# Kernel optimization log

Measured on AMD Instinct MI355X. Metric: run time of the kernel, lower is better.

Reference implementation:

```python
import jax, jax.numpy as jnp
import numpy as np

D_MODEL = 1024
NUM_HEADS = 16
D_K = D_MODEL // NUM_HEADS
SIM_THRESH = 0.7


def setup_inputs() -> dict:
    key = jax.random.key(0)
    ks = jax.random.split(key, 7)
    bs, seq = 2, 2048
    scale = 1.0 / np.sqrt(D_MODEL)
    x = jax.random.normal(ks[0], (bs, seq, D_MODEL), dtype=jnp.float32)
    Wq = jax.random.normal(ks[1], (D_MODEL, D_MODEL), dtype=jnp.float32) * scale
    Wk = jax.random.normal(ks[2], (D_MODEL, D_MODEL), dtype=jnp.float32) * scale
    Wv = jax.random.normal(ks[3], (D_MODEL, D_MODEL), dtype=jnp.float32) * scale
    bq = jax.random.normal(ks[4], (D_MODEL,), dtype=jnp.float32) * scale
    bk = jax.random.normal(ks[5], (D_MODEL,), dtype=jnp.float32) * scale
    bv = jax.random.normal(ks[6], (D_MODEL,), dtype=jnp.float32) * scale
    return {"x": x, "Wq": Wq, "bq": bq, "Wk": Wk, "bk": bk, "Wv": Wv, "bv": bv}


def reference(x, Wq, bq, Wk, bk, Wv, bv):
    bs, seq, d_model = x.shape
    # dynamic structural mask: cosine similarity > 0.7, shared across heads
    norm_x = x / jnp.maximum(jnp.linalg.norm(x, axis=-1, keepdims=True), 1e-12)
    sim = jnp.einsum('bsd,btd->bst', norm_x, norm_x)          # [B,S,S]
    mask = (sim > SIM_THRESH)[:, None, :, :]                  # [B,1,S,S]

    def proj(W, b):
        y = x @ W.T + b                                        # [B,S,D]
        return y.reshape(bs, seq, NUM_HEADS, D_K).transpose(0, 2, 1, 3)  # [B,H,S,dk]

    q = proj(Wq, bq)
    k = proj(Wk, bk)
    v = proj(Wv, bv)

    scores = jnp.einsum('bhsd,bhtd->bhst', q, k) / jnp.sqrt(jnp.float32(D_K))
    scores = jnp.where(mask, scores, -jnp.inf)
    attn = jax.nn.softmax(scores, axis=-1)                     # diag always unmasked
    return jnp.einsum('bhst,bhtd->bhsd', attn, v)              # [B,H,S,dk]
```

## Files before the change

kernel.cpp:

```cpp
#include <hip/hip_runtime.h>
#include <stdint.h>
#include <math.h>

#define D_MODEL 1024
#define NUM_HEADS 16
#define D_K 64
#define SEQ 2048
#define BATCH 2
#define SIM_THRESH 0.7f

#define TS 64
#define BK 32
#define NIT (D_MODEL / BK)

#define NROWS (BATCH * SEQ)
#define VP_BLOCKS ((NROWS / TS) * (D_MODEL / TS))
#define SIM_ROWB (SEQ / TS)
#define SIM_TRI (SIM_ROWB * (SIM_ROWB + 1) / 2)
#define SIM_BLOCKS (SIM_TRI * BATCH)
#define GRID (VP_BLOCKS + SIM_BLOCKS)

#define TILE_SH (TS * BK)

typedef __attribute__((ext_vector_type(8))) short bf16x8;
typedef __attribute__((ext_vector_type(4))) float f32x4;

static __device__ __forceinline__ unsigned short f2bf(float f) {
    unsigned int u = __float_as_uint(f);
    unsigned int r = (u + 0x7FFF + ((u >> 16) & 1)) >> 16;
    return (unsigned short)r;
}
static __device__ __forceinline__ float bf2f(unsigned short u) {
    return __uint_as_float(((unsigned int)u) << 16);
}

__global__ __launch_bounds__(256) void k_prep(const float* __restrict__ x,
                                              const float* __restrict__ Wv,
                                              unsigned short* __restrict__ xn,
                                              unsigned short* __restrict__ Wvb,
                                              float* __restrict__ norms,
                                              int* __restrict__ cnt) {
    int bid = blockIdx.x, tid = threadIdx.x;
    if (bid < NROWS) {
        const float4* xr = (const float4*)(x + (size_t)bid * D_MODEL);
        float4 vv = xr[tid];
        float ss = vv.x * vv.x + vv.y * vv.y + vv.z * vv.z + vv.w * vv.w;
        for (int off = 32; off > 0; off >>= 1) ss += __shfl_down(ss, off, 64);
        __shared__ float wsum[4];
        int lane = tid & 63, wv = tid >> 6;
        if (lane == 0) wsum[wv] = ss;
        __syncthreads();
        float nrm = sqrtf(wsum[0] + wsum[1] + wsum[2] + wsum[3]);
        float inv = 1.0f / fmaxf(nrm, 1e-12f);
        ushort4 o;
        o.x = f2bf(vv.x * inv); o.y = f2bf(vv.y * inv);
        o.z = f2bf(vv.z * inv); o.w = f2bf(vv.w * inv);
        *(ushort4*)(xn + (size_t)bid * D_MODEL + tid * 4) = o;
        if (tid == 0) { norms[bid] = nrm; cnt[bid] = 0; }
    } else {
        size_t i = (size_t)(bid - NROWS) * 256 + tid;
        float4 w = ((const float4*)Wv)[i];
        ushort4 o;
        o.x = f2bf(w.x); o.y = f2bf(w.y); o.z = f2bf(w.z); o.w = f2bf(w.w);
        *(ushort4*)(Wvb + i * 4) = o;
    }
}

static __device__ __forceinline__ void stage64x32(const unsigned short* __restrict__ gsrc,
                                                  int rowBase, int kk,
                                                  short* ldsDst, int tid) {
    int row = tid >> 2;
    int ch  = tid & 3;
    const unsigned short* ga = gsrc + (size_t)(rowBase + row) * D_MODEL + kk + ch * 8;
    __builtin_amdgcn_global_load_lds(
        (const __attribute__((address_space(1))) unsigned int*)ga,
        (__attribute__((address_space(3))) unsigned int*)(ldsDst + tid * 8),
        16, 0, 0);
}

__global__ __launch_bounds__(256) void k_main(const unsigned short* __restrict__ xn,
                                              const unsigned short* __restrict__ Wvb,
                                              const float* __restrict__ bv,
                                              const float* __restrict__ norms,
                                              float* __restrict__ v,
                                              int* __restrict__ cnt,
                                              float* __restrict__ out) {
    __shared__ short As[2 * TILE_SH];
    __shared__ short Bs[2 * TILE_SH];
    int bid = blockIdx.x;
    int tid = threadIdx.x;
    int lane = tid & 63, wave = tid >> 6;
    int wm = wave & 1, wn = wave >> 1;
    int lrow = lane & 15, quad = lane >> 4;

    const unsigned short* Asrc;
    const unsigned short* Bsrc;
    int rowBase, colBase;
    bool isV;
    int b = 0, bi = 0, bj = 0;
    if (bid < VP_BLOCKS) {
        isV = true;
        rowBase = (bid >> 4) * TS;
        colBase = (bid & 15) * TS;
        Asrc = xn;
        Bsrc = Wvb;
    } else {
        isV = false;
        int sidx = bid - VP_BLOCKS;
        b = (sidx >= SIM_TRI) ? 1 : 0;
        int r = sidx - b * SIM_TRI;
        bi = 0;
        while (r >= SIM_ROWB - bi) { r -= SIM_ROWB - bi; ++bi; }
        bj = bi + r;
        rowBase = bi * TS;
        colBase = bj * TS;
        Asrc = xn + (size_t)b * SEQ * D_MODEL;
        Bsrc = Asrc;
    }

    int aoff[2], boff[2];
#pragma unroll
    for (int i = 0; i < 2; ++i) {
        aoff[i] = (wm * 32 + i * 16 + lrow) * BK + quad * 8;
        boff[i] = (wn * 32 + i * 16 + lrow) * BK + quad * 8;
    }
    f32x4 acc[2][2] = {};

    stage64x32(Asrc, rowBase, 0, As, tid);
    stage64x32(Bsrc, colBase, 0, Bs, tid);
    __syncthreads();
    for (int it = 0; it < NIT; ++it) {
        int cur = it & 1, nxt = cur ^ 1;
        if (it + 1 < NIT) {
            stage64x32(Asrc, rowBase, (it + 1) * BK, As + nxt * TILE_SH, tid);
            stage64x32(Bsrc, colBase, (it + 1) * BK, Bs + nxt * TILE_SH, tid);
        }
        const short* Ac = As + cur * TILE_SH;
        const short* Bc = Bs + cur * TILE_SH;
        bf16x8 av[2], bvv[2];
#pragma unroll
        for (int i = 0; i < 2; ++i) av[i]  = *(const bf16x8*)(Ac + aoff[i]);
#pragma unroll
        for (int i = 0; i < 2; ++i) bvv[i] = *(const bf16x8*)(Bc + boff[i]);
#pragma unroll
        for (int mt = 0; mt < 2; ++mt)
#pragma unroll
            for (int nt = 0; nt < 2; ++nt)
                acc[mt][nt] = __builtin_amdgcn_mfma_f32_16x16x32_bf16(av[mt], bvv[nt], acc[mt][nt], 0, 0, 0);
        __syncthreads();
    }

    if (isV) {
#pragma unroll
        for (int mt = 0; mt < 2; ++mt) {
#pragma unroll
            for (int nt = 0; nt < 2; ++nt) {
                int n = colBase + wn * 32 + nt * 16 + lrow;
                float bn = bv[n];
                int h = n >> 6, j = n & 63;
#pragma unroll
                for (int r = 0; r < 4; ++r) {
                    int m = rowBase + wm * 32 + mt * 16 + quad * 4 + r;
                    float val = acc[mt][nt][r] * norms[m] + bn;
                    v[(size_t)m * D_MODEL + n] = val;
                    int bb = m >> 11, s = m & (SEQ - 1);
                    out[(((size_t)(bb * NUM_HEADS + h)) * SEQ + s) * D_K + j] = val;
                }
            }
        }
    } else {
        int* cb = cnt + b * SEQ;
        bool diag = (bi == bj);
#pragma unroll
        for (int mt = 0; mt < 2; ++mt) {
#pragma unroll
            for (int nt = 0; nt < 2; ++nt) {
                int n = colBase + wn * 32 + nt * 16 + lrow;
#pragma unroll
                for (int r = 0; r < 4; ++r) {
                    int m = rowBase + wm * 32 + mt * 16 + quad * 4 + r;
                    if (acc[mt][nt][r] > SIM_THRESH) {
                        atomicAdd(&cb[m], 1);
                        if (!diag) atomicAdd(&cb[n], 1);
                    }
                }
            }
        }
    }
}

__global__ __launch_bounds__(256) void k_fix(
    const float* __restrict__ x,
    const float* __restrict__ Wq, const float* __restrict__ bq,
    const float* __restrict__ Wk, const float* __restrict__ bk,
    const float* __restrict__ v,
    const unsigned short* __restrict__ xn,
    const int* __restrict__ cnt,
    float* __restrict__ out)
{
    int tid = threadIdx.x;
    int rowBase = blockIdx.x * 256;

    __shared__ int list[256];
    __shared__ int nlist;
    if (tid == 0) nlist = 0;
    __syncthreads();
    int grow = rowBase + tid;
    if (cnt[grow] != 1) { int p = atomicAdd(&nlist, 1); list[p] = grow; }
    __syncthreads();
    int nfix = nlist;
    if (nfix == 0) return;

    __shared__ uint8_t mrow[SEQ];
    __shared__ float q_row[D_MODEL];
    __shared__ float k_row[D_MODEL];
    __shared__ float accO[D_MODEL];
    __shared__ float m_h[NUM_HEADS], l_h[NUM_HEADS], alpha_h[NUM_HEADS], p_h[NUM_HEADS];

    for (int li = 0; li < nfix; ++li) {
        int row = list[li];
        int b = row >> 11, s = row & (SEQ - 1);

        const unsigned short* xs = xn + (size_t)row * D_MODEL;
        for (int t = tid; t < SEQ; t += 256) {
            const unsigned short* xt = xn + ((size_t)b * SEQ + t) * D_MODEL;
            float d = 0.f;
            for (int k = 0; k < D_MODEL; ++k) d += bf2f(xs[k]) * bf2f(xt[k]);
            mrow[t] = (d > SIM_THRESH) ? 1 : 0;
        }

        const float* xrow = x + (size_t)row * D_MODEL;
        for (int c = tid; c < D_MODEL; c += 256) {
            const float* w = Wq + (size_t)c * D_MODEL;
            float acc = bq[c];
            for (int d = 0; d < D_MODEL; ++d) acc += xrow[d] * w[d];
            q_row[c] = acc;
            accO[c] = 0.f;
        }
        if (tid < NUM_HEADS) { m_h[tid] = -INFINITY; l_h[tid] = 0.f; }
        __syncthreads();

        for (int t = 0; t < SEQ; ++t) {
            if (!mrow[t]) continue;
            const float* xt = x + ((size_t)b * SEQ + t) * D_MODEL;
            for (int c = tid; c < D_MODEL; c += 256) {
                const float* w = Wk + (size_t)c * D_MODEL;
                float acc = bk[c];
                for (int d = 0; d < D_MODEL; ++d) acc += xt[d] * w[d];
                k_row[c] = acc;
            }
            __syncthreads();
            if (tid < NUM_HEADS) {
                float sc = 0.f;
                for (int j = 0; j < D_K; ++j) sc += q_row[tid * D_K + j] * k_row[tid * D_K + j];
                sc *= 0.125f;
                float mnew = fmaxf(m_h[tid], sc);
                float alpha = expf(m_h[tid] - mnew);
                float p = expf(sc - mnew);
                l_h[tid] = l_h[tid] * alpha + p;
                m_h[tid] = mnew;
                alpha_h[tid] = alpha;
                p_h[tid] = p;
            }
            __syncthreads();
            const float* vt = v + ((size_t)b * SEQ + t) * D_MODEL;
            for (int c = tid; c < D_MODEL; c += 256) {
                int h = c >> 6;
                accO[c] = accO[c] * alpha_h[h] + p_h[h] * vt[c];
            }
            __syncthreads();
        }
        for (int c = tid; c < D_MODEL; c += 256) {
            int h = c >> 6, j = c & 63;
            out[(((size_t)(b * NUM_HEADS + h)) * SEQ + s) * D_K + j] = accO[c] / l_h[h];
        }
        __syncthreads();
    }
}

extern "C" void kernel_launch(void* const* d_in, const int* in_sizes, int n_in,
                              void* d_out, int out_size, void* d_ws, size_t ws_size,
                              hipStream_t stream) {
    const float* x  = (const float*)d_in[0];
    const float* Wq = (const float*)d_in[1];
    const float* bq = (const float*)d_in[2];
    const float* Wk = (const float*)d_in[3];
    const float* bk = (const float*)d_in[4];
    const float* Wv = (const float*)d_in[5];
    const float* bv = (const float*)d_in[6];
    float* out = (float*)d_out;

    unsigned short* xn  = (unsigned short*)d_ws;
    unsigned short* Wvb = xn + (size_t)NROWS * D_MODEL;
    float* v     = (float*)(Wvb + (size_t)D_MODEL * D_MODEL);
    float* norms = v + (size_t)NROWS * D_MODEL;
    int* cnt     = (int*)(norms + NROWS);

    k_prep<<<NROWS + D_MODEL * D_MODEL / 1024, 256, 0, stream>>>(x, Wv, xn, Wvb, norms, cnt);

    k_main<<<GRID, 256, 0, stream>>>(xn, Wvb, bv, norms, v, cnt, out);

    k_fix<<<NROWS / 256, 256, 0, stream>>>(x, Wq, bq, Wk, bk, v, xn, cnt, out);
}
```

Baseline: 126.1 us.

## Enlarge GEMM tiles to 128x128 and drop global V buffer write

Raises the output tile of the fused V-projection/similarity kernel from 64x64 to 128x128, with each wave computing a 4x4 grid of MFMA tiles. This improves operand reuse per LDS load and cuts the block count. The kernel no longer writes the full V matrix to global memory; the rare fix-up path now recomputes V rows from x and Wv alongside K. The costs are higher register pressure, fewer blocks for load balancing, and extra work in the fix-up path whenever rows need it.

```diff
diff --git a/kernel.cpp b/kernel.cpp
--- a/kernel.cpp
+++ b/kernel.cpp
@@ -9,7 +9,7 @@
 #define BATCH 2
 #define SIM_THRESH 0.7f
 
-#define TS 64
+#define TS 128
 #define BK 32
 #define NIT (D_MODEL / BK)
 
@@ -66,23 +66,25 @@
     }
 }
 
-static __device__ __forceinline__ void stage64x32(const unsigned short* __restrict__ gsrc,
-                                                  int rowBase, int kk,
-                                                  short* ldsDst, int tid) {
-    int row = tid >> 2;
-    int ch  = tid & 3;
-    const unsigned short* ga = gsrc + (size_t)(rowBase + row) * D_MODEL + kk + ch * 8;
-    __builtin_amdgcn_global_load_lds(
-        (const __attribute__((address_space(1))) unsigned int*)ga,
-        (__attribute__((address_space(3))) unsigned int*)(ldsDst + tid * 8),
-        16, 0, 0);
+static __device__ __forceinline__ void stage128x32(const unsigned short* __restrict__ gsrc,
+                                                   int kk, short* ldsDst, int tid) {
+#pragma unroll
+    for (int i = 0; i < 2; ++i) {
+        int c   = i * 256 + tid;
+        int row = c >> 2;
+        int ch  = c & 3;
+        const unsigned short* ga = gsrc + (size_t)row * D_MODEL + kk + ch * 8;
+        __builtin_amdgcn_global_load_lds(
+            (const __attribute__((address_space(1))) unsigned int*)ga,
+            (__attribute__((address_space(3))) unsigned int*)(ldsDst + c * 8),
+            16, 0, 0);
+    }
 }
 
 __global__ __launch_bounds__(256) void k_main(const unsigned short* __restrict__ xn,
                                               const unsigned short* __restrict__ Wvb,
                                               const float* __restrict__ bv,
                                               const float* __restrict__ norms,
-                                              float* __restrict__ v,
                                               int* __restrict__ cnt,
                                               float* __restrict__ out) {
     __shared__ short As[2 * TILE_SH];
@@ -100,10 +102,10 @@
     int b = 0, bi = 0, bj = 0;
     if (bid < VP_BLOCKS) {
         isV = true;
-        rowBase = (bid >> 4) * TS;
-        colBase = (bid & 15) * TS;
-        Asrc = xn;
-        Bsrc = Wvb;
+        rowBase = (bid >> 3) * TS;
+        colBase = (bid & 7) * TS;
+        Asrc = xn + (size_t)rowBase * D_MODEL;
+        Bsrc = Wvb + (size_t)colBase * D_MODEL;
     } else {
         isV = false;
         int sidx = bid - VP_BLOCKS;
@@ -114,55 +116,55 @@
         bj = bi + r;
         rowBase = bi * TS;
         colBase = bj * TS;
-        Asrc = xn + (size_t)b * SEQ * D_MODEL;
-        Bsrc = Asrc;
-    }
-
-    int aoff[2], boff[2];
-#pragma unroll
-    for (int i = 0; i < 2; ++i) {
-        aoff[i] = (wm * 32 + i * 16 + lrow) * BK + quad * 8;
-        boff[i] = (wn * 32 + i * 16 + lrow) * BK + quad * 8;
-    }
-    f32x4 acc[2][2] = {};
-
-    stage64x32(Asrc, rowBase, 0, As, tid);
-    stage64x32(Bsrc, colBase, 0, Bs, tid);
+        const unsigned short* base = xn + (size_t)b * SEQ * D_MODEL;
+        Asrc = base + (size_t)rowBase * D_MODEL;
+        Bsrc = base + (size_t)colBase * D_MODEL;
+    }
+
+    int aoff[4], boff[4];
+#pragma unroll
+    for (int i = 0; i < 4; ++i) {
+        aoff[i] = (wm * 64 + i * 16 + lrow) * BK + quad * 8;
+        boff[i] = (wn * 64 + i * 16 + lrow) * BK + quad * 8;
+    }
+    f32x4 acc[4][4] = {};
+
+    stage128x32(Asrc, 0, As, tid);
+    stage128x32(Bsrc, 0, Bs, tid);
     __syncthreads();
     for (int it = 0; it < NIT; ++it) {
         int cur = it & 1, nxt = cur ^ 1;
         if (it + 1 < NIT) {
-            stage64x32(Asrc, rowBase, (it + 1) * BK, As + nxt * TILE_SH, tid);
-            stage64x32(Bsrc, colBase, (it + 1) * BK, Bs + nxt * TILE_SH, tid);
+            stage128x32(Asrc, (it + 1) * BK, As + nxt * TILE_SH, tid);
+            stage128x32(Bsrc, (it + 1) * BK, Bs + nxt * TILE_SH, tid);
         }
         const short* Ac = As + cur * TILE_SH;
         const short* Bc = Bs + cur * TILE_SH;
-        bf16x8 av[2], bvv[2];
-#pragma unroll
-        for (int i = 0; i < 2; ++i) av[i]  = *(const bf16x8*)(Ac + aoff[i]);
-#pragma unroll
-        for (int i = 0; i < 2; ++i) bvv[i] = *(const bf16x8*)(Bc + boff[i]);
-#pragma unroll
-        for (int mt = 0; mt < 2; ++mt)
-#pragma unroll
-            for (int nt = 0; nt < 2; ++nt)
+        bf16x8 av[4], bvv[4];
+#pragma unroll
+        for (int i = 0; i < 4; ++i) av[i]  = *(const bf16x8*)(Ac + aoff[i]);
+#pragma unroll
+        for (int i = 0; i < 4; ++i) bvv[i] = *(const bf16x8*)(Bc + boff[i]);
+#pragma unroll
+        for (int mt = 0; mt < 4; ++mt)
+#pragma unroll
+            for (int nt = 0; nt < 4; ++nt)
                 acc[mt][nt] = __builtin_amdgcn_mfma_f32_16x16x32_bf16(av[mt], bvv[nt], acc[mt][nt], 0, 0, 0);
         __syncthreads();
     }
 
     if (isV) {
 #pragma unroll
-        for (int mt = 0; mt < 2; ++mt) {
-#pragma unroll
-            for (int nt = 0; nt < 2; ++nt) {
-                int n = colBase + wn * 32 + nt * 16 + lrow;
-                float bn = bv[n];
-                int h = n >> 6, j = n & 63;
+        for (int nt = 0; nt < 4; ++nt) {
+            int n = colBase + wn * 64 + nt * 16 + lrow;
+            float bn = bv[n];
+            int h = n >> 6, j = n & 63;
+#pragma unroll
+            for (int mt = 0; mt < 4; ++mt) {
 #pragma unroll
                 for (int r = 0; r < 4; ++r) {
-                    int m = rowBase + wm * 32 + mt * 16 + quad * 4 + r;
+                    int m = rowBase + wm * 64 + mt * 16 + quad * 4 + r;
                     float val = acc[mt][nt][r] * norms[m] + bn;
-                    v[(size_t)m * D_MODEL + n] = val;
                     int bb = m >> 11, s = m & (SEQ - 1);
                     out[(((size_t)(bb * NUM_HEADS + h)) * SEQ + s) * D_K + j] = val;
                 }
@@ -172,13 +174,13 @@
         int* cb = cnt + b * SEQ;
         bool diag = (bi == bj);
 #pragma unroll
-        for (int mt = 0; mt < 2; ++mt) {
-#pragma unroll
-            for (int nt = 0; nt < 2; ++nt) {
-                int n = colBase + wn * 32 + nt * 16 + lrow;
+        for (int nt = 0; nt < 4; ++nt) {
+            int n = colBase + wn * 64 + nt * 16 + lrow;
+#pragma unroll
+            for (int mt = 0; mt < 4; ++mt) {
 #pragma unroll
                 for (int r = 0; r < 4; ++r) {
-                    int m = rowBase + wm * 32 + mt * 16 + quad * 4 + r;
+                    int m = rowBase + wm * 64 + mt * 16 + quad * 4 + r;
                     if (acc[mt][nt][r] > SIM_THRESH) {
                         atomicAdd(&cb[m], 1);
                         if (!diag) atomicAdd(&cb[n], 1);
@@ -193,7 +195,7 @@
     const float* __restrict__ x,
     const float* __restrict__ Wq, const float* __restrict__ bq,
     const float* __restrict__ Wk, const float* __restrict__ bk,
-    const float* __restrict__ v,
+    const float* __restrict__ Wv, const float* __restrict__ bv,
     const unsigned short* __restrict__ xn,
     const int* __restrict__ cnt,
     float* __restrict__ out)
@@ -214,6 +216,7 @@
     __shared__ uint8_t mrow[SEQ];
     __shared__ float q_row[D_MODEL];
     __shared__ float k_row[D_MODEL];
+    __shared__ float v_row[D_MODEL];
     __shared__ float accO[D_MODEL];
     __shared__ float m_h[NUM_HEADS], l_h[NUM_HEADS], alpha_h[NUM_HEADS], p_h[NUM_HEADS];
 
@@ -244,10 +247,16 @@
             if (!mrow[t]) continue;
             const float* xt = x + ((size_t)b * SEQ + t) * D_MODEL;
             for (int c = tid; c < D_MODEL; c += 256) {
-                const float* w = Wk + (size_t)c * D_MODEL;
-                float acc = bk[c];
-                for (int d = 0; d < D_MODEL; ++d) acc += xt[d] * w[d];
-                k_row[c] = acc;
+                const float* wk = Wk + (size_t)c * D_MODEL;
+                const float* wv = Wv + (size_t)c * D_MODEL;
+                float ak = bk[c], av = bv[c];
+                for (int d = 0; d < D_MODEL; ++d) {
+                    float xv = xt[d];
+                    ak += xv * wk[d];
+                    av += xv * wv[d];
+                }
+                k_row[c] = ak;
+                v_row[c] = av;
             }
             __syncthreads();
             if (tid < NUM_HEADS) {
@@ -263,10 +272,9 @@
                 p_h[tid] = p;
             }
             __syncthreads();
-            const float* vt = v + ((size_t)b * SEQ + t) * D_MODEL;
             for (int c = tid; c < D_MODEL; c += 256) {
                 int h = c >> 6;
-                accO[c] = accO[c] * alpha_h[h] + p_h[h] * vt[c];
+                accO[c] = accO[c] * alpha_h[h] + p_h[h] * v_row[c];
             }
             __syncthreads();
         }
@@ -292,13 +300,12 @@
 
     unsigned short* xn  = (unsigned short*)d_ws;
     unsigned short* Wvb = xn + (size_t)NROWS * D_MODEL;
-    float* v     = (float*)(Wvb + (size_t)D_MODEL * D_MODEL);
-    float* norms = v + (size_t)NROWS * D_MODEL;
+    float* norms = (float*)(Wvb + (size_t)D_MODEL * D_MODEL);
     int* cnt     = (int*)(norms + NROWS);
 
     k_prep<<<NROWS + D_MODEL * D_MODEL / 1024, 256, 0, stream>>>(x, Wv, xn, Wvb, norms, cnt);
 
-    k_main<<<GRID, 256, 0, stream>>>(xn, Wvb, bv, norms, v, cnt, out);
-
-    k_fix<<<NROWS / 256, 256, 0, stream>>>(x, Wq, bq, Wk, bk, v, xn, cnt, out);
-}
+    k_main<<<GRID, 256, 0, stream>>>(xn, Wvb, bv, norms, cnt, out);
+
+    k_fix<<<NROWS / 256, 256, 0, stream>>>(x, Wq, bq, Wk, bk, Wv, bv, xn, cnt, out);
+}
```

Result: slower. 134.8 us (+6.9%).
